# Kernel optimization log

Measured on AMD Instinct MI355X. Metric: run time of the kernel, lower is better.

## Reference

```python
import jax, jax.numpy as jnp
import numpy as np

V, D, NH, NL, HID = 128000, 512, 8, 2, 1408
HD = D // NH
HALF = HD // 2
B, T, NLAB, LBL = 4, 508, 5, 4
EPS = 1e-5


def setup_inputs() -> dict:
    key = jax.random.key(0)
    ks = jax.random.split(key, 16)
    g = lambda k, sh: (jax.random.normal(k, sh, jnp.float32) * 0.02)
    return {
        "input_ids": jax.random.randint(ks[0], (B, T), 0, V),
        "label_ids": jax.random.randint(ks[1], (NLAB, LBL), 0, V),
        "emb": g(ks[2], (V, D)),
        "wq": g(ks[3], (NL, D, D)),
        "wk": g(ks[4], (NL, D, D)),
        "wv": g(ks[5], (NL, D, D)),
        "wo": g(ks[6], (NL, D, D)),
        "w1": g(ks[7], (NL, D, HID)),
        "w2": g(ks[8], (NL, HID, D)),
        "w3": g(ks[9], (NL, D, HID)),
        "attn_norm_w": jnp.ones((NL, D), jnp.float32),
        "ffn_norm_w": jnp.ones((NL, D), jnp.float32),
        "final_norm_w": jnp.ones((D,), jnp.float32),
        "lm_head": g(ks[10], (D, V)),
    }


def _rmsnorm(x, w):
    return x * jax.lax.rsqrt(jnp.mean(x * x, axis=-1, keepdims=True) + EPS) * w


def _score(input_ids, label_ids, emb, wq, wk, wv, wo, w1, w2, w3,
           attn_norm_w, ffn_norm_w, final_norm_w, lm_head):
    Bc, Tc = input_ids.shape
    nl, Lc = label_ids.shape
    S = Tc + Lc
    # pad_id is None in the original (tokenizer attr missing) -> all lengths == T.
    # Causal attention => one forward over [prefix || label] equals the per-token re-forwards.
    ctx = jnp.concatenate([
        jnp.broadcast_to(input_ids[None], (nl, Bc, Tc)),
        jnp.broadcast_to(label_ids[:, None, :], (nl, Bc, Lc)),
    ], axis=-1).reshape(nl * Bc, S)
    N = nl * Bc

    h = emb[ctx]  # [N, S, D]

    # RoPE tables
    pos = jnp.arange(S, dtype=jnp.float32)
    freqs = 1.0 / (10000.0 ** (jnp.arange(HALF, dtype=jnp.float32) / HALF))
    ang = pos[:, None] * freqs[None, :]  # [S, HALF]
    cos = jnp.cos(ang)[None, :, None, :]
    sin = jnp.sin(ang)[None, :, None, :]

    def rope(x):  # x: [N, S, NH, HD]
        x1, x2 = x[..., :HALF], x[..., HALF:]
        return jnp.concatenate([x1 * cos - x2 * sin, x1 * sin + x2 * cos], axis=-1)

    causal = jnp.tril(jnp.ones((S, S), dtype=bool))
    scale = 1.0 / jnp.sqrt(jnp.float32(HD))

    for l in range(NL):
        xn = _rmsnorm(h, attn_norm_w[l])
        q = rope((xn @ wq[l]).reshape(N, S, NH, HD))
        k = rope((xn @ wk[l]).reshape(N, S, NH, HD))
        v = (xn @ wv[l]).reshape(N, S, NH, HD)
        scores = jnp.einsum('nqhd,nkhd->nhqk', q, k) * scale
        scores = jnp.where(causal, scores, jnp.float32(-1e9))
        p = jax.nn.softmax(scores, axis=-1)
        o = jnp.einsum('nhqk,nkhd->nqhd', p, v).reshape(N, S, D)
        h = h + o @ wo[l]
        xn = _rmsnorm(h, ffn_norm_w[l])
        h = h + (jax.nn.silu(xn @ w1[l]) * (xn @ w3[l])) @ w2[l]

    h = _rmsnorm(h, final_norm_w)
    # Only positions T-1 .. T+L-2 predict label tokens; project only those.
    hs = h[:, Tc - 1:Tc - 1 + Lc, :]                    # [N, L, D]
    lp = jax.nn.log_softmax(hs @ lm_head, axis=-1)      # [N, L, V]
    lp = lp.reshape(nl, Bc, Lc, V)
    idx = jnp.broadcast_to(label_ids[:, None, :, None], (nl, Bc, Lc, 1))
    tok_lp = jnp.take_along_axis(lp, idx, axis=-1)[..., 0]  # [nl, B, L]
    return tok_lp.sum(axis=-1).T.astype(jnp.float32)        # [B, num_labels]


def reference(input_ids, label_ids, emb, wq, wk, wv, wo, w1, w2, w3,
              attn_norm_w, ffn_norm_w, final_norm_w, lm_head):
    return _score(input_ids, label_ids, emb, wq, wk, wv, wo, w1, w2, w3,
                  attn_norm_w, ffn_norm_w, final_norm_w, lm_head)
```

## Files before the change

### kernel.cpp

```cpp
#include <hip/hip_runtime.h>
#include <math.h>

typedef unsigned short u16;
typedef unsigned int u32;

namespace {
constexpr int kV = 128000, kD = 512, kNH = 8, kNL = 2, kHID = 1408;
constexpr int kHD = 64, kB = 4, kT = 508, kNLAB = 5, kLBL = 4;
constexpr int kS = 512;
constexpr int kNSeq = kNLAB * kB;
constexpr int kNS = kNSeq * kS;
constexpr int kQKV = 1536;
constexpr float kEps = 1e-5f;
constexpr int kNChunk = 2000;
constexpr int kPad = 56;
constexpr int kStr = 72;
constexpr int kPL = 3211264;
constexpr int oWQ = 0, oWK = 262144, oWV = 524288, oWO = 786432;
constexpr int oW1 = 1048576, oW3 = 1769472, oW2 = 2490368;
}

typedef __attribute__((ext_vector_type(8))) short bf16x8;
typedef __attribute__((ext_vector_type(4))) float f32x4;

__device__ inline u32 pk2(float lo, float hi) {
  u32 ul = __builtin_bit_cast(u32, lo);
  u32 uh = __builtin_bit_cast(u32, hi);
  ul += 0x7fffu + ((ul >> 16) & 1u);
  uh += 0x7fffu + ((uh >> 16) & 1u);
  return (ul >> 16) | (uh & 0xffff0000u);
}
__device__ inline u16 bf1(float x) {
  u32 u = __builtin_bit_cast(u32, x);
  u += 0x7fffu + ((u >> 16) & 1u);
  return (u16)(u >> 16);
}
__device__ inline float bf2f(u16 u) {
  return __builtin_bit_cast(float, ((u32)u) << 16);
}
__device__ inline void gload16(const void* g, void* l) {
  __builtin_amdgcn_global_load_lds(
      (const __attribute__((address_space(1))) void*)g,
      (__attribute__((address_space(3))) void*)l, 16, 0, 0);
}
__device__ inline size_t tix(int Kt, int row, int k) {
  return ((size_t)(row >> 7) * Kt + (k >> 6)) * 8192 +
         ((((k >> 4) & 3) * 2 + ((k >> 3) & 1)) * 128 + (row & 127)) * 8 + (k & 7);
}

__global__ __launch_bounds__(256) void k_wtrans_all(const float* __restrict__ wq,
                                                    const float* __restrict__ wk,
                                                    const float* __restrict__ wv,
                                                    const float* __restrict__ wo,
                                                    const float* __restrict__ w1,
                                                    const float* __restrict__ w3,
                                                    const float* __restrict__ w2,
                                                    u16* __restrict__ wT) {
  int bid = blockIdx.x;
  int l = bid / 3136, r = bid % 3136;
  const float* src; u16* dst; int K, N, gxw, t; float scale = 1.f;
  if (r < 1024) {
    int w = r >> 8; t = r & 255; K = 512; N = 512; gxw = 16;
    src = (w == 0 ? wq : w == 1 ? wk : w == 2 ? wv : wo) + (size_t)l * 262144;
    dst = wT + (size_t)l * kPL + w * 262144;
    if (w == 0) scale = 0.125f;
  } else if (r < 2432) {
    int rr = r - 1024; int w = rr / 704; t = rr - w * 704; K = 512; N = 1408; gxw = 44;
    src = (w ? w3 : w1) + (size_t)l * 720896;
    dst = wT + (size_t)l * kPL + (w ? oW3 : oW1);
  } else {
    t = r - 2432; K = 1408; N = 512; gxw = 16;
    src = w2 + (size_t)l * 720896;
    dst = wT + (size_t)l * kPL + oW2;
  }
  int bn = (t % gxw) * 32, bk = (t / gxw) * 32;
  __shared__ float tb[32][33];
  int tid = threadIdx.x;
  int rr2 = tid >> 3, c4 = (tid & 7) * 4;
  float4 v = *(const float4*)(src + (size_t)(bk + rr2) * N + bn + c4);
  tb[rr2][c4 + 0] = v.x * scale; tb[rr2][c4 + 1] = v.y * scale;
  tb[rr2][c4 + 2] = v.z * scale; tb[rr2][c4 + 3] = v.w * scale;
  __syncthreads();
  uint2 o;
  o.x = pk2(tb[c4 + 0][rr2], tb[c4 + 1][rr2]);
  o.y = pk2(tb[c4 + 2][rr2], tb[c4 + 3][rr2]);
  *(uint2*)&dst[tix(K >> 6, bn + rr2, bk + c4)] = o;
}

__global__ void k_embed(const int* __restrict__ input_ids, const int* __restrict__ label_ids,
                        const float* __restrict__ emb, float* __restrict__ h) {
  int row = blockIdx.x;
  int n = row / kS, s = row - n * kS;
  int lab = n / kB, b = n - lab * kB;
  int tok = (s < kT) ? input_ids[b * kT + s] : label_ids[lab * kLBL + (s - kT)];
  const float4* src = (const float4*)(emb + (size_t)tok * kD);
  float4* dst = (float4*)(h + (size_t)row * kD);
  for (int i = threadIdx.x; i < kD / 4; i += blockDim.x) dst[i] = src[i];
}

__global__ __launch_bounds__(256) void k_rmsnorm(const float* __restrict__ x,
                                                 const float* __restrict__ w,
                                                 u16* __restrict__ y) {
  int row = blockIdx.x;
  int tid = threadIdx.x;
  const float* xr = x + (size_t)row * kD;
  int i = tid * 2;
  float v0 = xr[i], v1 = xr[i + 1];
  float ss = v0 * v0 + v1 * v1;
  #pragma unroll
  for (int o = 1; o < 64; o <<= 1) ss += __shfl_xor(ss, o);
  __shared__ float wsum[4];
  int lane = tid & 63, wid = tid >> 6;
  if (lane == 0) wsum[wid] = ss;
  __syncthreads();
  float tot = wsum[0] + wsum[1] + wsum[2] + wsum[3];
  float inv = rsqrtf(tot / (float)kD + kEps);
  *(u32*)&y[tix(8, row, i)] = pk2(v0 * inv * w[i], v1 * inv * w[i + 1]);
}

__global__ __launch_bounds__(256) void k_gemm_qkv(const u16* __restrict__ A,
                                                  const u16* __restrict__ Bt,
                                                  u16* __restrict__ qkv) {
  __shared__ u16 As[8192];
  __shared__ u16 Bs[8192];
  int wg = (blockIdx.x & 7) * 120 + (blockIdx.x >> 3);
  int by = wg / 12, bx = wg - by * 12;
  int row0 = by * 128, col0 = bx * 128;
  int tid = threadIdx.x;
  int wave = tid >> 6, lane = tid & 63;
  int wm = wave >> 1, wn = wave & 1;
  int l15 = lane & 15, l16 = lane >> 4;
  f32x4 acc[4][4];
  #pragma unroll
  for (int i = 0; i < 4; i++)
    #pragma unroll
    for (int j = 0; j < 4; j++) acc[i][j] = (f32x4){0.f, 0.f, 0.f, 0.f};

  for (int kt = 0; kt < 8; kt++) {
    const u16* Ab = A  + ((size_t)(row0 >> 7) * 8 + kt) * 8192;
    const u16* Bb = Bt + ((size_t)(col0 >> 7) * 8 + kt) * 8192;
    #pragma unroll
    for (int i = 0; i < 4; i++) {
      int off = ((wave * 2 + (i >> 1)) * 128 + (i & 1) * 64) * 8;
      gload16(Ab + off + (size_t)lane * 8, (char*)As + off * 2);
      gload16(Bb + off + (size_t)lane * 8, (char*)Bs + off * 2);
    }
    __syncthreads();
    #pragma unroll
    for (int h = 0; h < 2; h++) {
      bf16x8 af[4], bfr[4];
      #pragma unroll
      for (int mf = 0; mf < 4; mf++)
        af[mf] = *(const bf16x8*)&As[((h * 4 + l16) * 128 + wm * 64 + mf * 16 + l15) * 8];
      #pragma unroll
      for (int nf = 0; nf < 4; nf++)
        bfr[nf] = *(const bf16x8*)&Bs[((h * 4 + l16) * 128 + wn * 64 + nf * 16 + l15) * 8];
      #pragma unroll
      for (int mf = 0; mf < 4; mf++)
        #pragma unroll
        for (int nf = 0; nf < 4; nf++)
          acc[mf][nf] = __builtin_amdgcn_mfma_f32_16x16x32_bf16(af[mf], bfr[nf], acc[mf][nf], 0, 0, 0);
    }
    __syncthreads();
  }

  if (bx < 8) {
    #pragma unroll
    for (int nf = 0; nf < 2; nf++) {
      int d = nf * 16 + l15;
      float fr = __expf(-0.2878231366242558f * (float)d);
      #pragma unroll
      for (int mf = 0; mf < 4; mf++)
        #pragma unroll
        for (int r = 0; r < 4; r++) {
          int row = row0 + wm * 64 + mf * 16 + l16 * 4 + r;
          int s = row & (kS - 1);
          float sn, cs;
          __sincosf((float)s * fr, &sn, &cs);
          float x1 = acc[mf][nf][r], x2 = acc[mf][nf + 2][r];
          size_t base = (size_t)row * kQKV + col0 + wn * 64 + nf * 16 + l15;
          qkv[base]      = bf1(x1 * cs - x2 * sn);
          qkv[base + 32] = bf1(x1 * sn + x2 * cs);
        }
    }
  } else {
    #pragma unroll
    for (int mf = 0; mf < 4; mf++)
      #pragma unroll
      for (int nf = 0; nf < 4; nf++)
        #pragma unroll
        for (int r = 0; r < 4; r++) {
          int row = row0 + wm * 64 + mf * 16 + l16 * 4 + r;
          qkv[(size_t)row * kQKV + col0 + wn * 64 + nf * 16 + l15] = bf1(acc[mf][nf][r]);
        }
  }
}

__global__ __launch_bounds__(256) void k_gemm_n64(const u16* __restrict__ A,
                                                  const u16* __restrict__ Bt,
                                                  float* __restrict__ C,
                                                  int Kt, int N) {
  __shared__ u16 As[8192];
  __shared__ u16 Bs[4096];
  int nwg = gridDim.x;
  int wg = (blockIdx.x & 7) * (nwg >> 3) + (blockIdx.x >> 3);
  int by = wg >> 3, bx = wg & 7;
  int row0 = by * 128, col0 = bx * 64;
  int p = col0 >> 7, half = (col0 >> 6) & 1;
  int tid = threadIdx.x;
  int wave = tid >> 6, lane = tid & 63;
  int l15 = lane & 15, l16 = lane >> 4;
  f32x4 acc[2][4];
  #pragma unroll
  for (int i = 0; i < 2; i++)
    #pragma unroll
    for (int j = 0; j < 4; j++) acc[i][j] = (f32x4){0.f, 0.f, 0.f, 0.f};

  for (int kt = 0; kt < Kt; kt++) {
    const u16* Ab = A  + ((size_t)(row0 >> 7) * Kt + kt) * 8192;
    const u16* Bb = Bt + ((size_t)p * Kt + kt) * 8192;
    #pragma unroll
    for (int i = 0; i < 4; i++) {
      int off = ((wave * 2 + (i >> 1)) * 128 + (i & 1) * 64) * 8;
      gload16(Ab + off + (size_t)lane * 8, (char*)As + off * 2);
    }
    #pragma unroll
    for (int sl = 0; sl < 2; sl++) {
      int ch = wave * 2 + sl;
      gload16(Bb + (ch * 128 + half * 64) * 8 + (size_t)lane * 8,
              (char*)Bs + (ch * 64) * 16);
    }
    __syncthreads();
    #pragma unroll
    for (int h = 0; h < 2; h++) {
      bf16x8 af[2], bfr[4];
      #pragma unroll
      for (int mf = 0; mf < 2; mf++)
        af[mf] = *(const bf16x8*)&As[((h * 4 + l16) * 128 + wave * 32 + mf * 16 + l15) * 8];
      #pragma unroll
      for (int nf = 0; nf < 4; nf++)
        bfr[nf] = *(const bf16x8*)&Bs[((h * 4 + l16) * 64 + nf * 16 + l15) * 8];
      #pragma unroll
      for (int mf = 0; mf < 2; mf++)
        #pragma unroll
        for (int nf = 0; nf < 4; nf++)
          acc[mf][nf] = __builtin_amdgcn_mfma_f32_16x16x32_bf16(af[mf], bfr[nf], acc[mf][nf], 0, 0, 0);
    }
    __syncthreads();
  }
  #pragma unroll
  for (int mf = 0; mf < 2; mf++)
    #pragma unroll
    for (int nf = 0; nf < 4; nf++)
      #pragma unroll
      for (int r = 0; r < 4; r++) {
        int row = row0 + wave * 32 + mf * 16 + l16 * 4 + r;
        int col = col0 + nf * 16 + l15;
        C[(size_t)row * N + col] += acc[mf][nf][r];
      }
}

__global__ __launch_bounds__(256) void k_ffn13_bf16(const u16* __restrict__ A,
                                                    const u16* __restrict__ W1t,
                                                    const u16* __restrict__ W3t,
                                                    u16* __restrict__ act) {
  __shared__ u16 As[8192];
  __shared__ u16 B1[8192];
  __shared__ u16 B2[8192];
  int wg = (blockIdx.x & 7) * 110 + (blockIdx.x >> 3);
  int by = wg / 11, bx = wg - by * 11;
  int row0 = by * 128, col0 = bx * 128;
  int tid = threadIdx.x;
  int wave = tid >> 6, lane = tid & 63;
  int wm = wave >> 1, wn = wave & 1;
  int l15 = lane & 15, l16 = lane >> 4;
  f32x4 acc1[4][4], acc2[4][4];
  #pragma unroll
  for (int i = 0; i < 4; i++)
    #pragma unroll
    for (int j = 0; j < 4; j++) {
      acc1[i][j] = (f32x4){0.f, 0.f, 0.f, 0.f};
      acc2[i][j] = (f32x4){0.f, 0.f, 0.f, 0.f};
    }

  for (int kt = 0; kt < 8; kt++) {
    const u16* Ab  = A   + ((size_t)(row0 >> 7) * 8 + kt) * 8192;
    const u16* B1b = W1t + ((size_t)(col0 >> 7) * 8 + kt) * 8192;
    const u16* B3b = W3t + ((size_t)(col0 >> 7) * 8 + kt) * 8192;
    #pragma unroll
    for (int i = 0; i < 4; i++) {
      int off = ((wave * 2 + (i >> 1)) * 128 + (i & 1) * 64) * 8;
      gload16(Ab  + off + (size_t)lane * 8, (char*)As + off * 2);
      gload16(B1b + off + (size_t)lane * 8, (char*)B1 + off * 2);
      gload16(B3b + off + (size_t)lane * 8, (char*)B2 + off * 2);
    }
    __syncthreads();
    #pragma unroll
    for (int h = 0; h < 2; h++) {
      bf16x8 af[4], b1f[4], b2f[4];
      #pragma unroll
      for (int mf = 0; mf < 4; mf++)
        af[mf] = *(const bf16x8*)&As[((h * 4 + l16) * 128 + wm * 64 + mf * 16 + l15) * 8];
      #pragma unroll
      for (int nf = 0; nf < 4; nf++) {
        b1f[nf] = *(const bf16x8*)&B1[((h * 4 + l16) * 128 + wn * 64 + nf * 16 + l15) * 8];
        b2f[nf] = *(const bf16x8*)&B2[((h * 4 + l16) * 128 + wn * 64 + nf * 16 + l15) * 8];
      }
      #pragma unroll
      for (int mf = 0; mf < 4; mf++)
        #pragma unroll
        for (int nf = 0; nf < 4; nf++) {
          acc1[mf][nf] = __builtin_amdgcn_mfma_f32_16x16x32_bf16(af[mf], b1f[nf], acc1[mf][nf], 0, 0, 0);
          acc2[mf][nf] = __builtin_amdgcn_mfma_f32_16x16x32_bf16(af[mf], b2f[nf], acc2[mf][nf], 0, 0, 0);
        }
    }
    __syncthreads();
  }
  #pragma unroll
  for (int mf = 0; mf < 4; mf++)
    #pragma unroll
    for (int nf = 0; nf < 4; nf++)
      #pragma unroll
      for (int r = 0; r < 4; r++) {
        int row = row0 + wm * 64 + mf * 16 + l16 * 4 + r;
        int col = col0 + wn * 64 + nf * 16 + l15;
        float aa = acc1[mf][nf][r];
        float sg = 1.f / (1.f + __expf(-aa));
        act[tix(22, row, col)] = bf1(aa * sg * acc2[mf][nf][r]);
      }
}

__global__ __launch_bounds__(256) void k_attn_mfma(const u16* __restrict__ qkv,
                                                   u16* __restrict__ o) {
  int qt = blockIdx.x;
  int nh = blockIdx.y;
  int hh = nh & (kNH - 1), n = nh >> 3;
  int tid = threadIdx.x;
  int wq = tid >> 6, lane = tid & 63;
  int l15 = lane & 15, l16 = lane >> 4;
  __shared__ u16 Ks[64 * kStr];
  __shared__ u16 Vt[64 * kStr];
  __shared__ u16 Ps[4][16 * kStr];
  int q0 = qt * 64;
  int qrow = q0 + wq * 16 + l15;

  bf16x8 qf[2];
  {
    const u16* qg = qkv + (size_t)(n * kS + qrow) * kQKV + hh * kHD;
    qf[0] = *(const bf16x8*)(qg + l16 * 8);
    qf[1] = *(const bf16x8*)(qg + 32 + l16 * 8);
  }

  f32x4 oacc[4];
  #pragma unroll
  for (int i = 0; i < 4; i++) oacc[i] = (f32x4){0.f, 0.f, 0.f, 0.f};
  float m_run = -1e30f, l_run = 0.f;

  int skv = tid & 63, sd0 = (tid >> 6) * 16;

  for (int jt = 0; jt <= qt; jt++) {
    int j0 = jt * 64;
    __syncthreads();
    {
      size_t gb = (size_t)(n * kS + j0 + skv) * kQKV + 512 + hh * kHD + sd0;
      const u16* kg = qkv + gb;
      *(uint4*)&Ks[skv * kStr + sd0]     = *(const uint4*)kg;
      *(uint4*)&Ks[skv * kStr + sd0 + 8] = *(const uint4*)(kg + 8);
      union { uint4 u4[2]; u16 us[16]; } vb;
      vb.u4[0] = *(const uint4*)(kg + 512);
      vb.u4[1] = *(const uint4*)(kg + 520);
      #pragma unroll
      for (int i = 0; i < 16; i++) Vt[(sd0 + i) * kStr + skv] = vb.us[i];
    }
    __syncthreads();

    f32x4 st[4];
    #pragma unroll
    for (int kt = 0; kt < 4; kt++) {
      bf16x8 ka0 = *(const bf16x8*)&Ks[(kt * 16 + l15) * kStr + l16 * 8];
      bf16x8 ka1 = *(const bf16x8*)&Ks[(kt * 16 + l15) * kStr + 32 + l16 * 8];
      f32x4 c = (f32x4){0.f, 0.f, 0.f, 0.f};
      c = __builtin_amdgcn_mfma_f32_16x16x32_bf16(ka0, qf[0], c, 0, 0, 0);
      c = __builtin_amdgcn_mfma_f32_16x16x32_bf16(ka1, qf[1], c, 0, 0, 0);
      st[kt] = c;
    }

    float mx = m_run;
    #pragma unroll
    for (int kt = 0; kt < 4; kt++)
      #pragma unroll
      for (int r = 0; r < 4; r++) {
        int kvg = j0 + kt * 16 + l16 * 4 + r;
        if (kvg > qrow) st[kt][r] = -1e30f;
        mx = fmaxf(mx, st[kt][r]);
      }
    mx = fmaxf(mx, __shfl_xor(mx, 16));
    mx = fmaxf(mx, __shfl_xor(mx, 32));
    float sc = __expf(m_run - mx);
    float p[4][4];
    float rs = 0.f;
    #pragma unroll
    for (int kt = 0; kt < 4; kt++)
      #pragma unroll
      for (int r = 0; r < 4; r++) { p[kt][r] = __expf(st[kt][r] - mx); rs += p[kt][r]; }
    rs += __shfl_xor(rs, 16);
    rs += __shfl_xor(rs, 32);
    l_run = l_run * sc + rs;
    m_run = mx;
    #pragma unroll
    for (int dt = 0; dt < 4; dt++)
      #pragma unroll
      for (int r = 0; r < 4; r++) oacc[dt][r] *= sc;

    #pragma unroll
    for (int kt = 0; kt < 4; kt++) {
      uint2 w2;
      w2.x = pk2(p[kt][0], p[kt][1]);
      w2.y = pk2(p[kt][2], p[kt][3]);
      *(uint2*)&Ps[wq][l15 * kStr + kt * 16 + l16 * 4] = w2;
    }
    asm volatile("s_waitcnt lgkmcnt(0)" ::: "memory");
    __builtin_amdgcn_sched_barrier(0);

    bf16x8 pf0 = *(const bf16x8*)&Ps[wq][l15 * kStr + l16 * 8];
    bf16x8 pf1 = *(const bf16x8*)&Ps[wq][l15 * kStr + 32 + l16 * 8];
    #pragma unroll
    for (int dt = 0; dt < 4; dt++) {
      bf16x8 va0 = *(const bf16x8*)&Vt[(dt * 16 + l15) * kStr + l16 * 8];
      bf16x8 va1 = *(const bf16x8*)&Vt[(dt * 16 + l15) * kStr + 32 + l16 * 8];
      oacc[dt] = __builtin_amdgcn_mfma_f32_16x16x32_bf16(va0, pf0, oacc[dt], 0, 0, 0);
      oacc[dt] = __builtin_amdgcn_mfma_f32_16x16x32_bf16(va1, pf1, oacc[dt], 0, 0, 0);
    }
  }

  float inv = 1.f / l_run;
  int rowIdx = n * kS + qrow;
  #pragma unroll
  for (int dt = 0; dt < 4; dt++) {
    uint2 ow;
    ow.x = pk2(oacc[dt][0] * inv, oacc[dt][1] * inv);
    ow.y = pk2(oacc[dt][2] * inv, oacc[dt][3] * inv);
    size_t base = ((size_t)(rowIdx >> 7) * 8 + hh) * 8192 +
                  (size_t)(((dt * 2 + ((l16 >> 1) & 1)) * 128 + (rowIdx & 127)) * 8 + (l16 & 1) * 4);
    *(uint2*)&o[base] = ow;
  }
}

__global__ __launch_bounds__(256) void k_rms_gather(const float* __restrict__ x,
                                                    const float* __restrict__ w,
                                                    u16* __restrict__ hs) {
  int r = blockIdx.x;
  int n = r >> 2, li = r & 3;
  int row = n * kS + (kT - 1 + li);
  int tid = threadIdx.x;
  const float* xr = x + (size_t)row * kD;
  int i = tid * 2;
  float v0 = xr[i], v1 = xr[i + 1];
  float ss = v0 * v0 + v1 * v1;
  #pragma unroll
  for (int o = 1; o < 64; o <<= 1) ss += __shfl_xor(ss, o);
  __shared__ float wsum[4];
  int lane = tid & 63, wid = tid >> 6;
  if (lane == 0) wsum[wid] = ss;
  __syncthreads();
  float tot = wsum[0] + wsum[1] + wsum[2] + wsum[3];
  float inv = rsqrtf(tot / (float)kD + kEps);
  *(u32*)&hs[(size_t)r * kD + i] = pk2(v0 * inv * w[i], v1 * inv * w[i + 1]);
}

__global__ __launch_bounds__(256) void k_logits_mfma(const u16* __restrict__ hs,
                                                     const float* __restrict__ lm,
                                                     float* __restrict__ part) {
  __shared__ u16 As[80 * kPad];
  __shared__ u16 Bs[256 * kPad];
  int tid = threadIdx.x;
  int wave = tid >> 6, lane = tid & 63;
  int l15 = lane & 15, l16 = lane >> 4;
  int col0 = blockIdx.x * 256;
  f32x4 acc[5][4];
  #pragma unroll
  for (int i = 0; i < 5; i++)
    #pragma unroll
    for (int j = 0; j < 4; j++) acc[i][j] = (f32x4){0.f, 0.f, 0.f, 0.f};

  int arow = tid >> 1, ahalf = tid & 1;
  int bkp = tid >> 4, bf4 = tid & 15;

  for (int k0 = 0; k0 < kD; k0 += 32) {
    if (tid < 160) {
      const u16* ag = hs + (size_t)arow * kD + k0 + ahalf * 16;
      *(uint4*)&As[arow * kPad + ahalf * 16]     = *(const uint4*)ag;
      *(uint4*)&As[arow * kPad + ahalf * 16 + 8] = *(const uint4*)(ag + 8);
    }
    #pragma unroll
    for (int t = 0; t < 4; t++) {
      int colq = bf4 + 16 * t;
      const float* bg = lm + (size_t)(k0 + 2 * bkp) * kV + col0 + colq * 4;
      float4 lo = *(const float4*)bg;
      float4 hi = *(const float4*)(bg + kV);
      *(u32*)&Bs[(colq * 4 + 0) * kPad + 2 * bkp] = pk2(lo.x, hi.x);
      *(u32*)&Bs[(colq * 4 + 1) * kPad + 2 * bkp] = pk2(lo.y, hi.y);
      *(u32*)&Bs[(colq * 4 + 2) * kPad + 2 * bkp] = pk2(lo.z, hi.z);
      *(u32*)&Bs[(colq * 4 + 3) * kPad + 2 * bkp] = pk2(lo.w, hi.w);
    }
    __syncthreads();
    bf16x8 af[5], bfr[4];
    #pragma unroll
    for (int mf = 0; mf < 5; mf++)
      af[mf] = *(const bf16x8*)&As[(mf * 16 + l15) * kPad + l16 * 8];
    #pragma unroll
    for (int nf = 0; nf < 4; nf++)
      bfr[nf] = *(const bf16x8*)&Bs[(wave * 64 + nf * 16 + l15) * kPad + l16 * 8];
    #pragma unroll
    for (int mf = 0; mf < 5; mf++)
      #pragma unroll
      for (int nf = 0; nf < 4; nf++)
        acc[mf][nf] = __builtin_amdgcn_mfma_f32_16x16x32_bf16(af[mf], bfr[nf], acc[mf][nf], 0, 0, 0);
    __syncthreads();
  }

  int chunk = blockIdx.x * 4 + wave;
  #pragma unroll
  for (int mf = 0; mf < 5; mf++)
    #pragma unroll
    for (int r = 0; r < 4; r++) {
      float mx = fmaxf(fmaxf(acc[mf][0][r], acc[mf][1][r]),
                       fmaxf(acc[mf][2][r], acc[mf][3][r]));
      #pragma unroll
      for (int off = 1; off < 16; off <<= 1) mx = fmaxf(mx, __shfl_xor(mx, off));
      float se = expf(acc[mf][0][r] - mx) + expf(acc[mf][1][r] - mx) +
                 expf(acc[mf][2][r] - mx) + expf(acc[mf][3][r] - mx);
      #pragma unroll
      for (int off = 1; off < 16; off <<= 1) se += __shfl_xor(se, off);
      if (l15 == 0) {
        int row = mf * 16 + l16 * 4 + r;
        size_t pi = ((size_t)row * kNChunk + chunk) * 2;
        part[pi] = mx; part[pi + 1] = se;
      }
    }
}

__global__ __launch_bounds__(64) void k_final(const float* __restrict__ part,
                                              const u16* __restrict__ hs,
                                              const float* __restrict__ lm,
                                              const int* __restrict__ label_ids,
                                              float* __restrict__ out) {
  int n = blockIdx.x;
  int lab = n / kB, b = n - lab * kB;
  int lane = threadIdx.x;
  float res = 0.f;
  for (int li = 0; li < kLBL; li++) {
    int r = n * kLBL + li;
    int tok = label_ids[lab * kLBL + li];
    float dv = 0.f;
    for (int d2 = lane; d2 < kD; d2 += 64)
      dv += bf2f(hs[(size_t)r * kD + d2]) * lm[(size_t)d2 * kV + tok];
    #pragma unroll
    for (int o2 = 1; o2 < 64; o2 <<= 1) dv += __shfl_xor(dv, o2);
    const float* pr = part + (size_t)r * kNChunk * 2;
    float mx = -1e30f;
    for (int c = lane; c < kNChunk; c += 64) mx = fmaxf(mx, pr[c * 2]);
    #pragma unroll
    for (int o2 = 1; o2 < 64; o2 <<= 1) mx = fmaxf(mx, __shfl_xor(mx, o2));
    float sum = 0.f;
    for (int c = lane; c < kNChunk; c += 64) sum += pr[c * 2 + 1] * expf(pr[c * 2] - mx);
    #pragma unroll
    for (int o2 = 1; o2 < 64; o2 <<= 1) sum += __shfl_xor(sum, o2);
    res += dv - (mx + logf(sum));
  }
  if (lane == 0) out[b * kNLAB + lab] = res;
}

extern "C" void kernel_launch(void* const* d_in, const int* in_sizes, int n_in,
                              void* d_out, int out_size, void* d_ws, size_t ws_size,
                              hipStream_t stream) {
  const int*   input_ids    = (const int*)d_in[0];
  const int*   label_ids    = (const int*)d_in[1];
  const float* emb          = (const float*)d_in[2];
  const float* wq           = (const float*)d_in[3];
  const float* wk           = (const float*)d_in[4];
  const float* wv           = (const float*)d_in[5];
  const float* wo           = (const float*)d_in[6];
  const float* w1           = (const float*)d_in[7];
  const float* w2           = (const float*)d_in[8];
  const float* w3           = (const float*)d_in[9];
  const float* attn_norm_w  = (const float*)d_in[10];
  const float* ffn_norm_w   = (const float*)d_in[11];
  const float* final_norm_w = (const float*)d_in[12];
  const float* lm_head      = (const float*)d_in[13];
  float* out = (float*)d_out;

  char* ws = (char*)d_ws;
  float* h    = (float*)(ws);
  u16*   xn   = (u16*)(ws + 20971520);
  u16*   qkv  = (u16*)(ws + 31457280);
  u16*   big  = (u16*)(ws + 62914560);
  u16*   hsb  = (u16*)(ws + 91750400);
  float* part = (float*)(ws + 91832320);
  u16*   wT   = (u16*)(ws + 93112640);

  k_wtrans_all<<<2 * 3136, 256, 0, stream>>>(wq, wk, wv, wo, w1, w3, w2, wT);
  k_embed<<<kNS, 128, 0, stream>>>(input_ids, label_ids, emb, h);

  for (int l = 0; l < kNL; l++) {
    u16* base = wT + (size_t)l * kPL;
    k_rmsnorm<<<kNS, 256, 0, stream>>>(h, attn_norm_w + (size_t)l * kD, xn);
    k_gemm_qkv<<<960, 256, 0, stream>>>(xn, base + oWQ, qkv);
    dim3 gattn(kS / 64, kNSeq * kNH);
    k_attn_mfma<<<gattn, 256, 0, stream>>>(qkv, big);
    k_gemm_n64<<<640, 256, 0, stream>>>(big, base + oWO, h, 8, kD);
    k_rmsnorm<<<kNS, 256, 0, stream>>>(h, ffn_norm_w + (size_t)l * kD, xn);
    k_ffn13_bf16<<<880, 256, 0, stream>>>(xn, base + oW1, base + oW3, big);
    k_gemm_n64<<<640, 256, 0, stream>>>(big, base + oW2, h, 22, kD);
  }

  k_rms_gather<<<kNSeq * kLBL, 256, 0, stream>>>(h, final_norm_w, hsb);
  k_logits_mfma<<<kV / 256, 256, 0, stream>>>(hsb, lm_head, part);
  k_final<<<kNSeq, 64, 0, stream>>>(part, hsb, lm_head, label_ids, out);
}
```

Before: 528.8 us.

## Write V pre-transposed from QKV GEMM and relayout logits B tile in LDS

```diff
diff --git a/kernel.cpp b/kernel.cpp
--- a/kernel.cpp
+++ b/kernel.cpp
@@ -10,7 +10,7 @@
 constexpr int kS = 512;
 constexpr int kNSeq = kNLAB * kB;
 constexpr int kNS = kNSeq * kS;
-constexpr int kQKV = 1536;
+constexpr int kQK = 1024;
 constexpr float kEps = 1e-5f;
 constexpr int kNChunk = 2000;
 constexpr int kPad = 56;
@@ -120,7 +120,8 @@
 
 __global__ __launch_bounds__(256) void k_gemm_qkv(const u16* __restrict__ A,
                                                   const u16* __restrict__ Bt,
-                                                  u16* __restrict__ qkv) {
+                                                  u16* __restrict__ qk,
+                                                  u16* __restrict__ vT) {
   __shared__ u16 As[8192];
   __shared__ u16 Bs[8192];
   int wg = (blockIdx.x & 7) * 120 + (blockIdx.x >> 3);
@@ -178,21 +179,26 @@
           float sn, cs;
           __sincosf((float)s * fr, &sn, &cs);
           float x1 = acc[mf][nf][r], x2 = acc[mf][nf + 2][r];
-          size_t base = (size_t)row * kQKV + col0 + wn * 64 + nf * 16 + l15;
-          qkv[base]      = bf1(x1 * cs - x2 * sn);
-          qkv[base + 32] = bf1(x1 * sn + x2 * cs);
+          size_t base = (size_t)row * kQK + col0 + wn * 64 + nf * 16 + l15;
+          qk[base]      = bf1(x1 * cs - x2 * sn);
+          qk[base + 32] = bf1(x1 * sn + x2 * cs);
         }
     }
   } else {
-    #pragma unroll
-    for (int mf = 0; mf < 4; mf++)
-      #pragma unroll
-      for (int nf = 0; nf < 4; nf++)
-        #pragma unroll
-        for (int r = 0; r < 4; r++) {
-          int row = row0 + wm * 64 + mf * 16 + l16 * 4 + r;
-          qkv[(size_t)row * kQKV + col0 + wn * 64 + nf * 16 + l15] = bf1(acc[mf][nf][r]);
-        }
+    int n = row0 >> 9;
+    #pragma unroll
+    for (int mf = 0; mf < 4; mf++) {
+      int s0 = (row0 & (kS - 1)) + wm * 64 + mf * 16 + l16 * 4;
+      #pragma unroll
+      for (int nf = 0; nf < 4; nf++) {
+        int v = (bx - 8) * 128 + wn * 64 + nf * 16 + l15;
+        int hh = v >> 6, d = v & 63;
+        uint2 ow;
+        ow.x = pk2(acc[mf][nf][0], acc[mf][nf][1]);
+        ow.y = pk2(acc[mf][nf][2], acc[mf][nf][3]);
+        *(uint2*)&vT[(size_t)((n * kNH + hh) * kHD + d) * kS + s0] = ow;
+      }
+    }
   }
 }
 
@@ -330,7 +336,8 @@
       }
 }
 
-__global__ __launch_bounds__(256) void k_attn_mfma(const u16* __restrict__ qkv,
+__global__ __launch_bounds__(256) void k_attn_mfma(const u16* __restrict__ qk,
+                                                   const u16* __restrict__ vT,
                                                    u16* __restrict__ o) {
   int qt = blockIdx.x;
   int nh = blockIdx.y;
@@ -346,7 +353,7 @@
 
   bf16x8 qf[2];
   {
-    const u16* qg = qkv + (size_t)(n * kS + qrow) * kQKV + hh * kHD;
+    const u16* qg = qk + (size_t)(n * kS + qrow) * kQK + hh * kHD;
     qf[0] = *(const bf16x8*)(qg + l16 * 8);
     qf[1] = *(const bf16x8*)(qg + 32 + l16 * 8);
   }
@@ -357,20 +364,19 @@
   float m_run = -1e30f, l_run = 0.f;
 
   int skv = tid & 63, sd0 = (tid >> 6) * 16;
+  const u16* vTh = vT + (size_t)((n * kNH + hh) * kHD) * kS;
 
   for (int jt = 0; jt <= qt; jt++) {
     int j0 = jt * 64;
     __syncthreads();
     {
-      size_t gb = (size_t)(n * kS + j0 + skv) * kQKV + 512 + hh * kHD + sd0;
-      const u16* kg = qkv + gb;
+      size_t gb = (size_t)(n * kS + j0 + skv) * kQK + 512 + hh * kHD + sd0;
+      const u16* kg = qk + gb;
       *(uint4*)&Ks[skv * kStr + sd0]     = *(const uint4*)kg;
       *(uint4*)&Ks[skv * kStr + sd0 + 8] = *(const uint4*)(kg + 8);
-      union { uint4 u4[2]; u16 us[16]; } vb;
-      vb.u4[0] = *(const uint4*)(kg + 512);
-      vb.u4[1] = *(const uint4*)(kg + 520);
-      #pragma unroll
-      for (int i = 0; i < 16; i++) Vt[(sd0 + i) * kStr + skv] = vb.us[i];
+      const u16* vg = vTh + (size_t)skv * kS + j0 + sd0;
+      *(uint4*)&Vt[skv * kStr + sd0]     = *(const uint4*)vg;
+      *(uint4*)&Vt[skv * kStr + sd0 + 8] = *(const uint4*)(vg + 8);
     }
     __syncthreads();
 
@@ -472,7 +478,7 @@
                                                      const float* __restrict__ lm,
                                                      float* __restrict__ part) {
   __shared__ u16 As[80 * kPad];
-  __shared__ u16 Bs[256 * kPad];
+  __shared__ u16 Bs[4 * 256 * 8];
   int tid = threadIdx.x;
   int wave = tid >> 6, lane = tid & 63;
   int l15 = lane & 15, l16 = lane >> 4;
@@ -485,6 +491,7 @@
 
   int arow = tid >> 1, ahalf = tid & 1;
   int bkp = tid >> 4, bf4 = tid & 15;
+  int slot = bkp >> 2, ksub = (2 * bkp) & 7;
 
   for (int k0 = 0; k0 < kD; k0 += 32) {
     if (tid < 160) {
@@ -498,10 +505,10 @@
       const float* bg = lm + (size_t)(k0 + 2 * bkp) * kV + col0 + colq * 4;
       float4 lo = *(const float4*)bg;
       float4 hi = *(const float4*)(bg + kV);
-      *(u32*)&Bs[(colq * 4 + 0) * kPad + 2 * bkp] = pk2(lo.x, hi.x);
-      *(u32*)&Bs[(colq * 4 + 1) * kPad + 2 * bkp] = pk2(lo.y, hi.y);
-      *(u32*)&Bs[(colq * 4 + 2) * kPad + 2 * bkp] = pk2(lo.z, hi.z);
-      *(u32*)&Bs[(colq * 4 + 3) * kPad + 2 * bkp] = pk2(lo.w, hi.w);
+      *(u32*)&Bs[(slot * 256 + colq * 4 + 0) * 8 + ksub] = pk2(lo.x, hi.x);
+      *(u32*)&Bs[(slot * 256 + colq * 4 + 1) * 8 + ksub] = pk2(lo.y, hi.y);
+      *(u32*)&Bs[(slot * 256 + colq * 4 + 2) * 8 + ksub] = pk2(lo.z, hi.z);
+      *(u32*)&Bs[(slot * 256 + colq * 4 + 3) * 8 + ksub] = pk2(lo.w, hi.w);
     }
     __syncthreads();
     bf16x8 af[5], bfr[4];
@@ -510,7 +517,7 @@
       af[mf] = *(const bf16x8*)&As[(mf * 16 + l15) * kPad + l16 * 8];
     #pragma unroll
     for (int nf = 0; nf < 4; nf++)
-      bfr[nf] = *(const bf16x8*)&Bs[(wave * 64 + nf * 16 + l15) * kPad + l16 * 8];
+      bfr[nf] = *(const bf16x8*)&Bs[(l16 * 256 + wave * 64 + nf * 16 + l15) * 8];
     #pragma unroll
     for (int mf = 0; mf < 5; mf++)
       #pragma unroll
@@ -593,7 +600,8 @@
   char* ws = (char*)d_ws;
   float* h    = (float*)(ws);
   u16*   xn   = (u16*)(ws + 20971520);
-  u16*   qkv  = (u16*)(ws + 31457280);
+  u16*   qk   = (u16*)(ws + 31457280);
+  u16*   vT   = (u16*)(ws + 52428800);
   u16*   big  = (u16*)(ws + 62914560);
   u16*   hsb  = (u16*)(ws + 91750400);
   float* part = (float*)(ws + 91832320);
@@ -605,9 +613,9 @@
   for (int l = 0; l < kNL; l++) {
     u16* base = wT + (size_t)l * kPL;
     k_rmsnorm<<<kNS, 256, 0, stream>>>(h, attn_norm_w + (size_t)l * kD, xn);
-    k_gemm_qkv<<<960, 256, 0, stream>>>(xn, base + oWQ, qkv);
+    k_gemm_qkv<<<960, 256, 0, stream>>>(xn, base + oWQ, qk, vT);
     dim3 gattn(kS / 64, kNSeq * kNH);
-    k_attn_mfma<<<gattn, 256, 0, stream>>>(qkv, big);
+    k_attn_mfma<<<gattn, 256, 0, stream>>>(qk, vT, big);
     k_gemm_n64<<<640, 256, 0, stream>>>(big, base + oWO, h, 8, kD);
     k_rmsnorm<<<kNS, 256, 0, stream>>>(h, ffn_norm_w + (size_t)l * kD, xn);
     k_ffn13_bf16<<<880, 256, 0, stream>>>(xn, base + oW1, base + oW3, big);
```

New measurement: 529.2 us. About the same (+0.1%).
